# Kernel optimization log

Measured on AMD Instinct MI355X. Metric: run time of the kernel, lower is better.

Reference implementation:

```python
import jax, jax.numpy as jnp
import numpy as np

SEQ = 2048
D_MODEL = 4096
N_HEADS = 16
D_HEAD = D_MODEL // N_HEADS
D_FF = 4 * D_MODEL


def setup_inputs() -> dict:
    key = jax.random.key(0)
    ks = jax.random.split(key, 8)
    s = 0.02
    return {
        "x": jax.random.normal(ks[0], (SEQ, D_MODEL), jnp.float32),
        "attn_bias": jax.random.normal(ks[1], (1, SEQ, SEQ), jnp.float32) * 0.1,
        "ln_scale": jnp.ones((D_MODEL,), jnp.float32),
        "ln_offset": jnp.zeros((D_MODEL,), jnp.float32),
        "wq": jax.random.normal(ks[2], (D_MODEL, D_MODEL), jnp.float32) * s,
        "wk": jax.random.normal(ks[3], (D_MODEL, D_MODEL), jnp.float32) * s,
        "wv": jax.random.normal(ks[4], (D_MODEL, D_MODEL), jnp.float32) * s,
        "wo": jax.random.normal(ks[5], (D_MODEL, D_MODEL), jnp.float32) * s,
        "w_ffn": jax.random.normal(ks[6], (D_MODEL, D_FF), jnp.float32) * s,
        "b_ffn": jnp.zeros((D_FF,), jnp.float32),
        "w_ffn_o": jax.random.normal(ks[7], (D_FF, D_MODEL), jnp.float32) * s,
        "b_ffn_o": jnp.zeros((D_MODEL,), jnp.float32),
    }


def reference(x, attn_bias, ln_scale, ln_offset, wq, wk, wv, wo,
              w_ffn, b_ffn, w_ffn_o, b_ffn_o):
    # ReplicatedLayerNorm (single shard: f_psum is identity)
    mean = jnp.mean(x, axis=-1, keepdims=True)
    var = jnp.var(x, axis=-1, keepdims=True)
    h = ln_scale * jax.lax.rsqrt(var + 1e-5) * (x - mean) + ln_offset

    seq = h.shape[0]
    q = (h @ wq).reshape(seq, N_HEADS, D_HEAD)
    k = (h @ wk).reshape(seq, N_HEADS, D_HEAD)
    v = (h @ wv).reshape(seq, N_HEADS, D_HEAD)

    logits = jnp.einsum('thd,Thd->htT', q, k) / np.float32(np.sqrt(D_HEAD))
    causal = jnp.tril(jnp.ones((seq, seq), jnp.float32))
    logits = logits - 1e10 * (1.0 - causal)
    logits = logits + attn_bias
    weights = jax.nn.softmax(logits, axis=-1)
    attn_vec = jnp.einsum('htT,Thd->thd', weights, v).reshape(seq, D_MODEL)
    attn_out = attn_vec @ wo

    # parallel GELU MLP on the same normed input
    ff = jax.nn.gelu(h @ w_ffn + b_ffn)
    dense_out = ff @ w_ffn_o + b_ffn_o

    return attn_out + dense_out
```

## Files before the change

kernel.cpp:

```cpp
#include <hip/hip_runtime.h>
#include <stdint.h>

#define SEQ 2048
#define DM 4096
#define NHEADS 16
#define DHEAD 256
#define DFF 16384

typedef __attribute__((ext_vector_type(8))) short short8;
typedef __attribute__((ext_vector_type(4))) float f32x4;
typedef __attribute__((ext_vector_type(4))) float float4v;
typedef __attribute__((ext_vector_type(4))) unsigned short ushort4v;
typedef __attribute__((ext_vector_type(8))) unsigned short ushort8v;

__device__ __forceinline__ unsigned short f2b(float f) {
    uint32_t u = __builtin_bit_cast(uint32_t, f);
    u = (u + 0x7FFFu + ((u >> 16) & 1u)) >> 16;
    return (unsigned short)u;
}

__device__ __forceinline__ void gload_lds16(const void* g, void* l) {
    __builtin_amdgcn_global_load_lds((const __attribute__((address_space(1))) void*)g,
                                     (__attribute__((address_space(3))) void*)l, 16, 0, 0);
}

template <typename T>
__global__ __launch_bounds__(256) void transpose_cvt(const T* __restrict__ src,
                                                     unsigned short* __restrict__ dst,
                                                     int ldS, int ldD, int R, int C) {
    __shared__ unsigned short tl[64 * 66];
    int r0 = blockIdx.y << 6, c0 = blockIdx.x << 6;
    int tid = threadIdx.x;
#pragma unroll
    for (int it = 0; it < 4; ++it) {
        int e = (tid + it * 256) * 4;
        int rr = e >> 6, cc = e & 63;
        const T* sp = src + (size_t)(r0 + rr) * ldS + c0 + cc;
        if constexpr (sizeof(T) == 4) {
            float4v v = *(const float4v*)sp;
#pragma unroll
            for (int j = 0; j < 4; ++j) tl[rr * 66 + cc + j] = f2b(v[j]);
        } else {
            ushort4v v = *(const ushort4v*)sp;
#pragma unroll
            for (int j = 0; j < 4; ++j) tl[rr * 66 + cc + j] = v[j];
        }
    }
    __syncthreads();
#pragma unroll
    for (int it = 0; it < 2; ++it) {
        int e = tid + it * 256;
        int oc = e >> 3;
        int k8 = (e & 7) * 8;
        ushort8v w;
#pragma unroll
        for (int j = 0; j < 8; ++j) w[j] = tl[(k8 + j) * 66 + oc];
        *(ushort8v*)(dst + (size_t)(c0 + oc) * ldD + r0 + k8) = w;
    }
}

__global__ __launch_bounds__(256) void ln_kernel(const float* __restrict__ x,
                                                 const float* __restrict__ sc,
                                                 const float* __restrict__ of,
                                                 unsigned short* __restrict__ h) {
    int row = blockIdx.x;
    int tid = threadIdx.x, lane = tid & 63, wave = tid >> 6;
    const float4v* xr = (const float4v*)(x + (size_t)row * DM);
    float4v v[4];
    float s = 0.f, s2 = 0.f;
#pragma unroll
    for (int i = 0; i < 4; ++i) {
        v[i] = xr[tid + i * 256];
#pragma unroll
        for (int j = 0; j < 4; ++j) { s += v[i][j]; s2 += v[i][j] * v[i][j]; }
    }
#pragma unroll
    for (int o = 1; o < 64; o <<= 1) { s += __shfl_xor(s, o); s2 += __shfl_xor(s2, o); }
    __shared__ float rs[4], rs2[4];
    if (lane == 0) { rs[wave] = s; rs2[wave] = s2; }
    __syncthreads();
    s = rs[0] + rs[1] + rs[2] + rs[3];
    s2 = rs2[0] + rs2[1] + rs2[2] + rs2[3];
    float mean = s * (1.0f / DM);
    float var = s2 * (1.0f / DM) - mean * mean;
    float inv = rsqrtf(var + 1e-5f);
#pragma unroll
    for (int i = 0; i < 4; ++i) {
        int c = (tid + i * 256) * 4;
        ushort4v o4;
#pragma unroll
        for (int j = 0; j < 4; ++j)
            o4[j] = f2b((v[i][j] - mean) * inv * sc[c + j] + of[c + j]);
        *(ushort4v*)(h + (size_t)row * DM + c) = o4;
    }
}

#define MF(a, b, c) __builtin_amdgcn_mfma_f32_16x16x32_bf16(a, b, c, 0, 0, 0)
#define FENCE() asm volatile("" ::: "memory")
#define LGKM0() asm volatile("s_waitcnt lgkmcnt(0)" ::: "memory")
#define BARR() __builtin_amdgcn_s_barrier()

#define RDA(BUF, MB)                                                                     \
    _Pragma("unroll") for (int i2 = 0; i2 < 4; ++i2) {                                   \
        af[i2][0] = *(const short8*)((BUF) + (arowb + ((MB) + i2) * 16) * 64 + ca0);     \
        af[i2][1] = *(const short8*)((BUF) + (arowb + ((MB) + i2) * 16) * 64 + ca1);     \
    }
#define RDB(BUF, NB)                                                                     \
    _Pragma("unroll") for (int j2 = 0; j2 < 2; ++j2) {                                   \
        bf[(NB) + j2][0] = *(const short8*)((BUF) + (brow + ((NB) + j2) * 16) * 64 + ca0);\
        bf[(NB) + j2][1] = *(const short8*)((BUF) + (brow + ((NB) + j2) * 16) * 64 + ca1);\
    }
#define MMQ(MB, NB)                                                                      \
    __builtin_amdgcn_s_setprio(1);                                                       \
    _Pragma("unroll") for (int kk = 0; kk < 2; ++kk)                                     \
        _Pragma("unroll") for (int i2 = 0; i2 < 4; ++i2)                                 \
            _Pragma("unroll") for (int j2 = 0; j2 < 2; ++j2)                             \
                acc[(MB) + i2][(NB) + j2] =                                              \
                    MF(af[i2][kk], bf[(NB) + j2][kk], acc[(MB) + i2][(NB) + j2]);        \
    __builtin_amdgcn_s_setprio(0)

template <int EPI, int SPLIT>
__global__ __launch_bounds__(512, 1) void gemm2sq(const unsigned short* __restrict__ A,
                                                  const unsigned short* __restrict__ BT,
                                                  void* __restrict__ Cout,
                                                  int M, int N, int Kfull, int ldc,
                                                  const float* __restrict__ bias) {
    __shared__ unsigned short aL[2][256 * 64];
    __shared__ unsigned short bL[2][256 * 64];

    const int nby = M >> 8, nbx = N >> 8;
    const int nwg = nby * nbx;
    int b = blockIdx.x;
    int sp = 0;
    if (SPLIT == 2) { sp = (b >= nwg) ? 1 : 0; b -= sp * nwg; }
    const int Keff = Kfull / SPLIT;
    const int koff = sp * Keff;

    const int slabw = nbx >> 3;
    const int xcd = b & 7;
    const int jj = b >> 3;
    const int bx = xcd * slabw + jj / nby;
    const int by = jj % nby;
    const int bm0 = by << 8, bn0 = bx << 8;

    const int tid = threadIdx.x, lane = tid & 63, wave = tid >> 6;
    const int wm = wave >> 2, wn = wave & 3;
    const int l15 = lane & 15, kl = lane >> 4;

    const int rh = tid >> 3;
    const int cb_s = (tid & 7) << 4;
    const int kx = (cb_s ^ ((rh & 7) << 4)) >> 1;

    const unsigned short* Abase = A + (size_t)(bm0 + rh) * Kfull + koff + kx;
    const unsigned short* Bbase = BT + (size_t)(bn0 + rh) * Kfull + koff + kx;

    auto stageA = [&](int v, int h) {
        const unsigned short* g = Abase + (size_t)v * 64 + (size_t)(h * 128) * Kfull;
        char* l = (char*)aL[v & 1] + h * 16384 + tid * 16;
        gload_lds16(g, l);
        gload_lds16(g + (size_t)64 * Kfull, l + 8192);
    };
    auto stageB = [&](int v, int h) {
        const unsigned short* g = Bbase + (size_t)v * 64 + (size_t)(h * 128) * Kfull;
        char* l = (char*)bL[v & 1] + h * 16384 + tid * 16;
        gload_lds16(g, l);
        gload_lds16(g + (size_t)64 * Kfull, l + 8192);
    };

    const int arowb = wm * 128 + l15;
    const int brow = wn * 64 + l15;
    const int sa = (l15 & 7) << 4;
    const int ca0 = ((kl * 16) ^ sa) >> 1;
    const int ca1 = ((64 + kl * 16) ^ sa) >> 1;

    f32x4 acc[8][4];
#pragma unroll
    for (int i = 0; i < 8; ++i)
#pragma unroll
        for (int j2 = 0; j2 < 4; ++j2) acc[i][j2] = (f32x4){0.f, 0.f, 0.f, 0.f};

    short8 af[4][2], bf[4][2];

    stageA(0, 0); stageA(0, 1); stageB(0, 0); stageB(0, 1); stageB(1, 0); stageB(1, 1);
    asm volatile("s_waitcnt vmcnt(4)" ::: "memory");
    BARR();

    const int NI = (Keff >> 6) >> 1;
    for (int t2 = 0; t2 < NI; ++t2) {
        const int u = t2 << 1;
        const bool last = (t2 == NI - 1);
        const unsigned short* a0 = aL[0];
        const unsigned short* b0 = bL[0];
        const unsigned short* a1 = aL[1];
        const unsigned short* b1 = bL[1];

        RDA(a0, 0); RDB(b0, 0);
        stageA(u + 1, 0);
        FENCE(); BARR();
        MMQ(0, 0);
        LGKM0(); BARR();
        RDB(b0, 2);
        stageA(u + 1, 1);
        FENCE(); BARR();
        MMQ(0, 2);
        LGKM0(); BARR();
        RDA(a0, 4);
        if (!last) stageB(u + 2, 0);
        FENCE(); BARR();
        MMQ(4, 0);
        LGKM0(); BARR();
        if (!last) stageB(u + 2, 1);
        FENCE(); BARR();
        MMQ(4, 2);
        if (last) { asm volatile("s_waitcnt vmcnt(0)" ::: "memory"); }
        else      { asm volatile("s_waitcnt vmcnt(4)" ::: "memory"); }
        LGKM0(); BARR();

        RDA(a1, 0); RDB(b1, 0);
        if (!last) stageA(u + 2, 0);
        FENCE(); BARR();
        MMQ(0, 0);
        LGKM0(); BARR();
        RDB(b1, 2);
        if (!last) stageA(u + 2, 1);
        FENCE(); BARR();
        MMQ(0, 2);
        LGKM0(); BARR();
        RDA(a1, 4);
        if (!last) stageB(u + 3, 0);
        FENCE(); BARR();
        MMQ(4, 0);
        LGKM0(); BARR();
        if (!last) stageB(u + 3, 1);
        FENCE(); BARR();
        MMQ(4, 2);
        if (!last) { asm volatile("s_waitcnt vmcnt(4)" ::: "memory"); }
        LGKM0(); BARR();
    }

    const int r0 = bm0 + wm * 128 + kl * 4;
    const int c0g = bn0 + wn * 64 + l15;
#pragma unroll
    for (int mi = 0; mi < 8; ++mi) {
#pragma unroll
        for (int nj = 0; nj < 4; ++nj) {
            int col = c0g + nj * 16;
#pragma unroll
            for (int r = 0; r < 4; ++r) {
                int row = r0 + mi * 16 + r;
                float v = acc[mi][nj][r];
                if constexpr (EPI == 0) {
                    ((unsigned short*)Cout)[(size_t)row * ldc + col] = f2b(v);
                } else if constexpr (EPI == 1) {
                    ((float*)Cout)[(size_t)sp * M * N + (size_t)row * ldc + col] = v;
                } else {
                    v += bias[col];
                    float t = tanhf(0.7978845608f * (v + 0.044715f * v * v * v));
                    ((unsigned short*)Cout)[(size_t)row * ldc + col] = f2b(0.5f * v * (1.0f + t));
                }
            }
        }
    }
}

__global__ __launch_bounds__(256) void final_reduce(const float* __restrict__ fp,
                                                    const float* __restrict__ wp,
                                                    const float* __restrict__ bias,
                                                    float* __restrict__ out) {
    size_t i = (size_t)blockIdx.x * 256 + threadIdx.x;
    const float4v* f0 = (const float4v*)fp;
    const float4v* f1 = (const float4v*)(fp + (size_t)SEQ * DM);
    const float4v* w0 = (const float4v*)wp;
    const float4v* w1 = (const float4v*)(wp + (size_t)SEQ * DM);
    const float4v* b4 = (const float4v*)bias;
    float4v v = f0[i] + f1[i] + w0[i] + w1[i] + b4[i & (DM / 4 - 1)];
    ((float4v*)out)[i] = v;
}

__global__ __launch_bounds__(256, 2) void attn_kernel(const unsigned short* __restrict__ qkv,
                                                      const unsigned short* __restrict__ vT,
                                                      const float* __restrict__ bias,
                                                      unsigned short* __restrict__ attn_vec) {
    __shared__ unsigned short kL[64 * 264];
    __shared__ unsigned short vL[256 * 72];
    __shared__ unsigned short pL[4][16 * 72];

    int qb = blockIdx.x, head = blockIdx.y;
    int tid = threadIdx.x, lane = tid & 63, wave = tid >> 6;
    int q16 = lane & 15, q4 = lane >> 4;

    short8 qf[8];
    {
        const unsigned short* qp =
            qkv + (size_t)(qb * 64 + wave * 16 + q16) * (3 * DM) + head * DHEAD + (q4 << 3);
#pragma unroll
        for (int kk = 0; kk < 8; ++kk) qf[kk] = *(const short8*)(qp + kk * 32);
    }

    f32x4 o[16];
#pragma unroll
    for (int d = 0; d < 16; ++d) o[d] = (f32x4){0.f, 0.f, 0.f, 0.f};
    float m_run[4] = {-INFINITY, -INFINITY, -INFINITY, -INFINITY};
    float l_run[4] = {0.f, 0.f, 0.f, 0.f};
    int qrow0 = qb * 64 + wave * 16 + q4 * 4;

    for (int t = 0; t <= qb; ++t) {
        int kv0 = t * 64;
#pragma unroll
        for (int rr = 0; rr < 8; ++rr) {
            int i = tid + rr * 256;
            int row = i >> 5, c8 = (i & 31) << 3;
            *(ushort8v*)(kL + row * 264 + c8) =
                *(const ushort8v*)(qkv + (size_t)(kv0 + row) * (3 * DM) + DM + head * DHEAD + c8);
        }
#pragma unroll
        for (int rr = 0; rr < 8; ++rr) {
            int i = tid + rr * 256;
            int d = i >> 3, c8 = (i & 7) << 3;
            *(ushort8v*)(vL + d * 72 + c8) =
                *(const ushort8v*)(vT + (size_t)(head * DHEAD + d) * SEQ + kv0 + c8);
        }
        __syncthreads();

        f32x4 s[4];
#pragma unroll
        for (int c = 0; c < 4; ++c) s[c] = (f32x4){0.f, 0.f, 0.f, 0.f};
#pragma unroll
        for (int kk = 0; kk < 8; ++kk) {
#pragma unroll
            for (int c = 0; c < 4; ++c) {
                short8 kf = *(const short8*)(kL + (c * 16 + q16) * 264 + kk * 32 + (q4 << 3));
                s[c] = __builtin_amdgcn_mfma_f32_16x16x32_bf16(qf[kk], kf, s[c], 0, 0, 0);
            }
        }

        bool diag = (t == qb);
#pragma unroll
        for (int r = 0; r < 4; ++r) {
            int qr = qrow0 + r;
            float sv[4];
#pragma unroll
            for (int c = 0; c < 4; ++c) {
                float vv = s[c][r] * 0.0625f + bias[(size_t)qr * SEQ + kv0 + c * 16 + q16];
                if (diag && (kv0 + c * 16 + q16) > qr) vv = -1e30f;
                sv[c] = vv;
            }
            float m = fmaxf(fmaxf(sv[0], sv[1]), fmaxf(sv[2], sv[3]));
#pragma unroll
            for (int off = 1; off < 16; off <<= 1) m = fmaxf(m, __shfl_xor(m, off));
            float mn = fmaxf(m_run[r], m);
            float alpha = __expf(m_run[r] - mn);
            float psum = 0.f;
#pragma unroll
            for (int c = 0; c < 4; ++c) {
                float p = __expf(sv[c] - mn);
                psum += p;
                pL[wave][(q4 * 4 + r) * 72 + c * 16 + q16] = f2b(p);
            }
#pragma unroll
            for (int off = 1; off < 16; off <<= 1) psum += __shfl_xor(psum, off);
            l_run[r] = l_run[r] * alpha + psum;
            m_run[r] = mn;
#pragma unroll
            for (int d = 0; d < 16; ++d) o[d][r] *= alpha;
        }

#pragma unroll
        for (int ks = 0; ks < 2; ++ks) {
            short8 pa = *(const short8*)(pL[wave] + q16 * 72 + ks * 32 + (q4 << 3));
#pragma unroll
            for (int d = 0; d < 16; ++d) {
                short8 vb = *(const short8*)(vL + (d * 16 + q16) * 72 + ks * 32 + (q4 << 3));
                o[d] = __builtin_amdgcn_mfma_f32_16x16x32_bf16(pa, vb, o[d], 0, 0, 0);
            }
        }
        __syncthreads();
    }

#pragma unroll
    for (int r = 0; r < 4; ++r) {
        float inv = 1.0f / l_run[r];
#pragma unroll
        for (int d = 0; d < 16; ++d)
            attn_vec[(size_t)(qrow0 + r) * DM + head * DHEAD + d * 16 + q16] = f2b(o[d][r] * inv);
    }
}

extern "C" void kernel_launch(void* const* d_in, const int* in_sizes, int n_in,
                              void* d_out, int out_size, void* d_ws, size_t ws_size,
                              hipStream_t stream) {
    const float* x = (const float*)d_in[0];
    const float* attn_bias = (const float*)d_in[1];
    const float* ln_scale = (const float*)d_in[2];
    const float* ln_offset = (const float*)d_in[3];
    const float* wq = (const float*)d_in[4];
    const float* wk = (const float*)d_in[5];
    const float* wv = (const float*)d_in[6];
    const float* wo = (const float*)d_in[7];
    const float* w_ffn = (const float*)d_in[8];
    const float* b_ffn = (const float*)d_in[9];
    const float* w_ffn_o = (const float*)d_in[10];
    const float* b_ffn_o = (const float*)d_in[11];
    float* out = (float*)d_out;

    char* p = (char*)d_ws;
    unsigned short* WT_qkv = (unsigned short*)p; p += (size_t)3 * DM * DM * 2;
    unsigned short* WT_o = (unsigned short*)p;   p += (size_t)DM * DM * 2;
    unsigned short* WT_f1 = (unsigned short*)p;  p += (size_t)DFF * DM * 2;
    unsigned short* WT_f2 = (unsigned short*)p;  p += (size_t)DM * DFF * 2;
    unsigned short* hB = (unsigned short*)p;     p += (size_t)SEQ * DM * 2;
    unsigned short* qkvB = (unsigned short*)p;   p += (size_t)SEQ * 3 * DM * 2;
    unsigned short* vTB = (unsigned short*)p;    p += (size_t)DM * SEQ * 2;
    unsigned short* avB = (unsigned short*)p;    p += (size_t)SEQ * DM * 2;
    unsigned short* ffB = (unsigned short*)p;    p += (size_t)SEQ * DFF * 2;

    float* fp = (float*)WT_qkv;
    float* wp = (float*)WT_f1;

    transpose_cvt<float><<<dim3(DM / 64, DM / 64), 256, 0, stream>>>(wq, WT_qkv, DM, DM, DM, DM);
    transpose_cvt<float><<<dim3(DM / 64, DM / 64), 256, 0, stream>>>(wk, WT_qkv + (size_t)DM * DM, DM, DM, DM, DM);
    transpose_cvt<float><<<dim3(DM / 64, DM / 64), 256, 0, stream>>>(wv, WT_qkv + (size_t)2 * DM * DM, DM, DM, DM, DM);
    transpose_cvt<float><<<dim3(DM / 64, DM / 64), 256, 0, stream>>>(wo, WT_o, DM, DM, DM, DM);
    transpose_cvt<float><<<dim3(DFF / 64, DM / 64), 256, 0, stream>>>(w_ffn, WT_f1, DFF, DM, DM, DFF);
    transpose_cvt<float><<<dim3(DM / 64, DFF / 64), 256, 0, stream>>>(w_ffn_o, WT_f2, DM, DFF, DFF, DM);

    ln_kernel<<<SEQ, 256, 0, stream>>>(x, ln_scale, ln_offset, hB);

    gemm2sq<0, 1><<<(SEQ / 256) * (3 * DM / 256), 512, 0, stream>>>(hB, WT_qkv, qkvB, SEQ, 3 * DM, DM, 3 * DM, nullptr);
    transpose_cvt<unsigned short><<<dim3(DM / 64, SEQ / 64), 256, 0, stream>>>(qkvB + 2 * DM, vTB, 3 * DM, SEQ, SEQ, DM);

    attn_kernel<<<dim3(SEQ / 64, NHEADS), 256, 0, stream>>>(qkvB, vTB, attn_bias, avB);

    gemm2sq<2, 1><<<(SEQ / 256) * (DFF / 256), 512, 0, stream>>>(hB, WT_f1, ffB, SEQ, DFF, DM, DFF, b_ffn);
    gemm2sq<1, 2><<<2 * (SEQ / 256) * (DM / 256), 512, 0, stream>>>(avB, WT_o, wp, SEQ, DM, DM, DM, nullptr);
    gemm2sq<1, 2><<<2 * (SEQ / 256) * (DM / 256), 512, 0, stream>>>(ffB, WT_f2, fp, SEQ, DM, DFF, DM, nullptr);
    final_reduce<<<(SEQ * DM / 4) / 256, 256, 0, stream>>>(fp, wp, b_ffn_o, out);
}
```

Before: 1.284 ms.

## Merge QKV and FFN-up GEMMs into one launch, restructure LDS reads, faster GELU

The QKV projection and the FFN up-projection share input h, so they now run as one grouped GEMM launch of 896 workgroups, with runtime epilogue selection replacing the template parameter. The main loop reads all 8 A fragments and 4 B fragments per K slice up front and drops the explicit lgkmcnt(0) waits, leaving the compiler to insert LDS waits. The GELU tanh is rewritten in the equivalent x*sigmoid(2z) form using __expf. These changes aim to cut launch and tail costs and loop stalls, at the price of more VGPRs and a runtime branch in the epilogue.

Result: faster. 1.249 ms (-2.7%).

```diff
diff --git a/kernel.cpp b/kernel.cpp
--- a/kernel.cpp
+++ b/kernel.cpp
@@ -97,18 +97,17 @@
 
 #define MF(a, b, c) __builtin_amdgcn_mfma_f32_16x16x32_bf16(a, b, c, 0, 0, 0)
 #define FENCE() asm volatile("" ::: "memory")
-#define LGKM0() asm volatile("s_waitcnt lgkmcnt(0)" ::: "memory")
 #define BARR() __builtin_amdgcn_s_barrier()
 
-#define RDA(BUF, MB)                                                                     \
+#define RDA4(BUF, MB)                                                                    \
     _Pragma("unroll") for (int i2 = 0; i2 < 4; ++i2) {                                   \
-        af[i2][0] = *(const short8*)((BUF) + (arowb + ((MB) + i2) * 16) * 64 + ca0);     \
-        af[i2][1] = *(const short8*)((BUF) + (arowb + ((MB) + i2) * 16) * 64 + ca1);     \
-    }
-#define RDB(BUF, NB)                                                                     \
-    _Pragma("unroll") for (int j2 = 0; j2 < 2; ++j2) {                                   \
-        bf[(NB) + j2][0] = *(const short8*)((BUF) + (brow + ((NB) + j2) * 16) * 64 + ca0);\
-        bf[(NB) + j2][1] = *(const short8*)((BUF) + (brow + ((NB) + j2) * 16) * 64 + ca1);\
+        af[(MB) + i2][0] = *(const short8*)((BUF) + (arowb + ((MB) + i2) * 16) * 64 + ca0);\
+        af[(MB) + i2][1] = *(const short8*)((BUF) + (arowb + ((MB) + i2) * 16) * 64 + ca1);\
+    }
+#define RDB4(BUF)                                                                        \
+    _Pragma("unroll") for (int j2 = 0; j2 < 4; ++j2) {                                   \
+        bf[j2][0] = *(const short8*)((BUF) + (brow + j2 * 16) * 64 + ca0);               \
+        bf[j2][1] = *(const short8*)((BUF) + (brow + j2 * 16) * 64 + ca1);               \
     }
 #define MMQ(MB, NB)                                                                      \
     __builtin_amdgcn_s_setprio(1);                                                       \
@@ -116,21 +115,33 @@
         _Pragma("unroll") for (int i2 = 0; i2 < 4; ++i2)                                 \
             _Pragma("unroll") for (int j2 = 0; j2 < 2; ++j2)                             \
                 acc[(MB) + i2][(NB) + j2] =                                              \
-                    MF(af[i2][kk], bf[(NB) + j2][kk], acc[(MB) + i2][(NB) + j2]);        \
+                    MF(af[(MB) + i2][kk], bf[(NB) + j2][kk], acc[(MB) + i2][(NB) + j2]); \
     __builtin_amdgcn_s_setprio(0)
 
-template <int EPI, int SPLIT>
-__global__ __launch_bounds__(512, 1) void gemm2sq(const unsigned short* __restrict__ A,
-                                                  const unsigned short* __restrict__ BT,
-                                                  void* __restrict__ Cout,
-                                                  int M, int N, int Kfull, int ldc,
-                                                  const float* __restrict__ bias) {
+template <int SPLIT>
+__global__ __launch_bounds__(512, 1) void gemm2sq(
+    const unsigned short* __restrict__ A, int M, int Kfull, int nwg0,
+    const unsigned short* __restrict__ BT_0, void* __restrict__ C_0, int N_0, int ldc_0,
+    const float* __restrict__ bias_0, int epi_0,
+    const unsigned short* __restrict__ BT_1, void* __restrict__ C_1, int N_1, int ldc_1,
+    const float* __restrict__ bias_1, int epi_1) {
     __shared__ unsigned short aL[2][256 * 64];
     __shared__ unsigned short bL[2][256 * 64];
 
+    int b = blockIdx.x;
+    const unsigned short* BT;
+    void* Cout;
+    int N, ldc, epi;
+    const float* bias;
+    if (b < nwg0) {
+        BT = BT_0; Cout = C_0; N = N_0; ldc = ldc_0; bias = bias_0; epi = epi_0;
+    } else {
+        b -= nwg0;
+        BT = BT_1; Cout = C_1; N = N_1; ldc = ldc_1; bias = bias_1; epi = epi_1;
+    }
+
     const int nby = M >> 8, nbx = N >> 8;
     const int nwg = nby * nbx;
-    int b = blockIdx.x;
     int sp = 0;
     if (SPLIT == 2) { sp = (b >= nwg) ? 1 : 0; b -= sp * nwg; }
     const int Keff = Kfull / SPLIT;
@@ -179,7 +190,7 @@
 #pragma unroll
         for (int j2 = 0; j2 < 4; ++j2) acc[i][j2] = (f32x4){0.f, 0.f, 0.f, 0.f};
 
-    short8 af[4][2], bf[4][2];
+    short8 af[8][2], bf[4][2];
 
     stageA(0, 0); stageA(0, 1); stageB(0, 0); stageB(0, 1); stageB(1, 0); stageB(1, 1);
     asm volatile("s_waitcnt vmcnt(4)" ::: "memory");
@@ -194,48 +205,46 @@
         const unsigned short* a1 = aL[1];
         const unsigned short* b1 = bL[1];
 
-        RDA(a0, 0); RDB(b0, 0);
+        RDA4(a0, 0); RDB4(b0);
         stageA(u + 1, 0);
         FENCE(); BARR();
         MMQ(0, 0);
-        LGKM0(); BARR();
-        RDB(b0, 2);
+        BARR();
+        RDA4(a0, 4);
         stageA(u + 1, 1);
         FENCE(); BARR();
         MMQ(0, 2);
-        LGKM0(); BARR();
-        RDA(a0, 4);
+        BARR();
         if (!last) stageB(u + 2, 0);
         FENCE(); BARR();
         MMQ(4, 0);
-        LGKM0(); BARR();
+        BARR();
         if (!last) stageB(u + 2, 1);
         FENCE(); BARR();
         MMQ(4, 2);
         if (last) { asm volatile("s_waitcnt vmcnt(0)" ::: "memory"); }
         else      { asm volatile("s_waitcnt vmcnt(4)" ::: "memory"); }
-        LGKM0(); BARR();
-
-        RDA(a1, 0); RDB(b1, 0);
+        BARR();
+
+        RDA4(a1, 0); RDB4(b1);
         if (!last) stageA(u + 2, 0);
         FENCE(); BARR();
         MMQ(0, 0);
-        LGKM0(); BARR();
-        RDB(b1, 2);
+        BARR();
+        RDA4(a1, 4);
         if (!last) stageA(u + 2, 1);
         FENCE(); BARR();
         MMQ(0, 2);
-        LGKM0(); BARR();
-        RDA(a1, 4);
+        BARR();
         if (!last) stageB(u + 3, 0);
         FENCE(); BARR();
         MMQ(4, 0);
-        LGKM0(); BARR();
+        BARR();
         if (!last) stageB(u + 3, 1);
         FENCE(); BARR();
         MMQ(4, 2);
         if (!last) { asm volatile("s_waitcnt vmcnt(4)" ::: "memory"); }
-        LGKM0(); BARR();
+        BARR();
     }
 
     const int r0 = bm0 + wm * 128 + kl * 4;
@@ -249,14 +258,15 @@
             for (int r = 0; r < 4; ++r) {
                 int row = r0 + mi * 16 + r;
                 float v = acc[mi][nj][r];
-                if constexpr (EPI == 0) {
+                if (epi == 0) {
                     ((unsigned short*)Cout)[(size_t)row * ldc + col] = f2b(v);
-                } else if constexpr (EPI == 1) {
+                } else if (epi == 1) {
                     ((float*)Cout)[(size_t)sp * M * N + (size_t)row * ldc + col] = v;
                 } else {
                     v += bias[col];
-                    float t = tanhf(0.7978845608f * (v + 0.044715f * v * v * v));
-                    ((unsigned short*)Cout)[(size_t)row * ldc + col] = f2b(0.5f * v * (1.0f + t));
+                    float z = 1.5957691216f * (v + 0.044715f * v * v * v);
+                    float g = v / (1.0f + __expf(-z));
+                    ((unsigned short*)Cout)[(size_t)row * ldc + col] = f2b(g);
                 }
             }
         }
@@ -426,13 +436,23 @@
 
     ln_kernel<<<SEQ, 256, 0, stream>>>(x, ln_scale, ln_offset, hB);
 
-    gemm2sq<0, 1><<<(SEQ / 256) * (3 * DM / 256), 512, 0, stream>>>(hB, WT_qkv, qkvB, SEQ, 3 * DM, DM, 3 * DM, nullptr);
+    gemm2sq<1><<<896, 512, 0, stream>>>(
+        hB, SEQ, DM, 384,
+        WT_qkv, qkvB, 3 * DM, 3 * DM, nullptr, 0,
+        WT_f1, ffB, DFF, DFF, b_ffn, 2);
+
     transpose_cvt<unsigned short><<<dim3(DM / 64, SEQ / 64), 256, 0, stream>>>(qkvB + 2 * DM, vTB, 3 * DM, SEQ, SEQ, DM);
 
     attn_kernel<<<dim3(SEQ / 64, NHEADS), 256, 0, stream>>>(qkvB, vTB, attn_bias, avB);
 
-    gemm2sq<2, 1><<<(SEQ / 256) * (DFF / 256), 512, 0, stream>>>(hB, WT_f1, ffB, SEQ, DFF, DM, DFF, b_ffn);
-    gemm2sq<1, 2><<<2 * (SEQ / 256) * (DM / 256), 512, 0, stream>>>(avB, WT_o, wp, SEQ, DM, DM, DM, nullptr);
-    gemm2sq<1, 2><<<2 * (SEQ / 256) * (DM / 256), 512, 0, stream>>>(ffB, WT_f2, fp, SEQ, DM, DFF, DM, nullptr);
+    gemm2sq<2><<<256, 512, 0, stream>>>(
+        avB, SEQ, DM, 256,
+        WT_o, wp, DM, DM, nullptr, 1,
+        nullptr, nullptr, DM, DM, nullptr, 1);
+    gemm2sq<2><<<256, 512, 0, stream>>>(
+        ffB, SEQ, DFF, 256,
+        WT_f2, fp, DM, DM, nullptr, 1,
+        nullptr, nullptr, DM, DM, nullptr, 1);
+
     final_reduce<<<(SEQ * DM / 4) / 256, 256, 0, stream>>>(fp, wp, b_ffn_o, out);
 }
```
